# Optimization experiments

Measured on AMD Instinct MI355X. Metric: run time of the kernel, lower is better.

Reference implementation:

```python
import jax, jax.numpy as jnp
import numpy as np

N_NODES = 50000
N_EDGES = 800000
D_IN = 128
D_OUT = 128


def setup_inputs() -> dict:
    key = jax.random.key(0)
    k1, k2, k3, k4 = jax.random.split(key, 4)
    feature = jax.random.normal(k1, (N_NODES, D_IN), dtype=jnp.float32)
    relation_indices = jax.random.randint(k2, (2, N_EDGES), 0, N_NODES, dtype=jnp.int64)
    relation_weight = jax.random.uniform(k3, (N_EDGES, 1), dtype=jnp.float32)
    W = jax.random.normal(k4, (2 * D_IN, D_OUT), dtype=jnp.float32) * (1.0 / np.sqrt(2 * D_IN))
    b = jnp.zeros((D_OUT,), dtype=jnp.float32)
    return {"feature": feature, "relation_indices": relation_indices,
            "relation_weight": relation_weight, "W": W, "b": b}


def reference(feature, relation_indices, relation_weight, W, b):
    dst = relation_indices[0]  # segment ids (aggregation target) [E]
    src = relation_indices[1]  # neighbor ids gathered from feature [E]
    # gather neighbor features and apply edge weights (dropout_rate=0 -> identity)
    feat_n = feature[src] * relation_weight  # [E, D_IN]
    # segment mean over destination nodes
    n = feature.shape[0]
    sums = jax.ops.segment_sum(feat_n, dst, num_segments=n)  # [N, D_IN]
    cnts = jax.ops.segment_sum(jnp.ones((feat_n.shape[0],), dtype=feat_n.dtype), dst, num_segments=n)
    neigh_mean = sums / jnp.maximum(cnts, 1.0)[:, None]
    # concat(self, mean_neighbor) -> linear update
    h = jnp.concatenate([feature, neigh_mean], axis=-1)  # [N, 2*D_IN]
    return h @ W + b  # [N, D_OUT]
```

## Files before the change

### kernel.cpp

```cpp
#include <hip/hip_runtime.h>
#include <hip/hip_bf16.h>
#include <stdint.h>

#define N_NODES 50000
#define N_EDGES 800000
#define D 128
#define K_DIM 256
#define NB_SCAN 196

typedef __attribute__((ext_vector_type(8))) short bf16x8;
typedef __attribute__((ext_vector_type(4))) float f32x4;

#define SUMS_OFF  0
#define WSW_OFF   25600000
#define HIST_OFF  25665536
#define OFFS_OFF  25865536
#define CURS_OFF  26065552
#define EDGE_OFF  26265552
#define BSUM_OFF  32665552
#define BOFF_OFF  32666576

__device__ inline short f2bf(float x) {
  union { float f; uint32_t u; } v; v.f = x;
  uint32_t r = v.u + 0x7FFFu + ((v.u >> 16) & 1u);
  return (short)(r >> 16);
}

__global__ __launch_bounds__(256) void k_wswz(const float* __restrict__ W,
                                              short* __restrict__ wsw) {
  int t = blockIdx.x * 256 + threadIdx.x;
  int kstep = t >> 9;
  int ntile = (t >> 6) & 7;
  int lane  = t & 63;
  int k0  = kstep * 32 + (lane >> 4) * 8;
  int col = ntile * 16 + (lane & 15);
  bf16x8 o;
  #pragma unroll
  for (int j = 0; j < 8; ++j) o[j] = f2bf(W[(k0 + j) * D + col]);
  *(bf16x8*)(wsw + t * 8) = o;
}

__global__ __launch_bounds__(256) void k_hist(const int* __restrict__ idx,
                                              int* __restrict__ hist) {
  int e = blockIdx.x * 256 + threadIdx.x;
  if (e < N_EDGES) atomicAdd(&hist[idx[e]], 1);
}

__global__ __launch_bounds__(256) void k_scan1(const int* __restrict__ hist,
                                               int* __restrict__ blockSum) {
  __shared__ int red[256];
  int t = threadIdx.x;
  int i = blockIdx.x * 256 + t;
  red[t] = (i < N_NODES) ? hist[i] : 0;
  __syncthreads();
  #pragma unroll
  for (int s = 128; s > 0; s >>= 1) {
    if (t < s) red[t] += red[t + s];
    __syncthreads();
  }
  if (t == 0) blockSum[blockIdx.x] = red[0];
}

__global__ __launch_bounds__(256) void k_scan2(const int* __restrict__ blockSum,
                                               int* __restrict__ blockOff,
                                               int* __restrict__ offs) {
  __shared__ int lds[256];
  int t = threadIdx.x;
  int v = (t < NB_SCAN) ? blockSum[t] : 0;
  lds[t] = v;
  __syncthreads();
  #pragma unroll
  for (int off = 1; off < 256; off <<= 1) {
    int add = (t >= off) ? lds[t - off] : 0;
    __syncthreads();
    lds[t] += add;
    __syncthreads();
  }
  if (t < NB_SCAN) blockOff[t] = lds[t] - v;
  if (t == 255) offs[N_NODES] = lds[255];
}

__global__ __launch_bounds__(256) void k_scan3(const int* __restrict__ hist,
                                               const int* __restrict__ blockOff,
                                               int* __restrict__ offs,
                                               int* __restrict__ cursor) {
  __shared__ int lds[256];
  int t = threadIdx.x;
  int i = blockIdx.x * 256 + t;
  int v = (i < N_NODES) ? hist[i] : 0;
  lds[t] = v;
  __syncthreads();
  #pragma unroll
  for (int off = 1; off < 256; off <<= 1) {
    int add = (t >= off) ? lds[t - off] : 0;
    __syncthreads();
    lds[t] += add;
    __syncthreads();
  }
  int excl = lds[t] - v + blockOff[blockIdx.x];
  if (i < N_NODES) { offs[i] = excl; cursor[i] = excl; }
}

__global__ __launch_bounds__(256) void k_scatter(const int* __restrict__ idx,
                                                 const float* __restrict__ w,
                                                 int* __restrict__ cursor,
                                                 int2* __restrict__ edge) {
  int e = blockIdx.x * 256 + threadIdx.x;
  if (e < N_EDGES) {
    int dst = idx[e];
    int p = atomicAdd(&cursor[dst], 1);
    union { float f; int i; } u; u.f = w[e];
    edge[p] = make_int2(idx[N_EDGES + e], u.i);
  }
}

__global__ __launch_bounds__(256) void k_agg(const float* __restrict__ feat,
                                             const int* __restrict__ offs,
                                             const int2* __restrict__ edge,
                                             float* __restrict__ sums) {
  int t = blockIdx.x * 256 + threadIdx.x;
  int node = t >> 5;
  int c = t & 31;
  if (node >= N_NODES) return;
  int beg = offs[node], end = offs[node + 1];
  f32x4 acc = (f32x4){0.f, 0.f, 0.f, 0.f};
  for (int j = beg; j < end; ++j) {
    int2 ed = edge[j];
    union { int i; float f; } u; u.i = ed.y;
    float wt = u.f;
    f32x4 f = *(const f32x4*)(feat + (size_t)ed.x * D + c * 4);
    acc.x += f.x * wt; acc.y += f.y * wt; acc.z += f.z * wt; acc.w += f.w * wt;
  }
  *(f32x4*)(sums + (size_t)node * D + c * 4) = acc;
}

__global__ __launch_bounds__(256) void k_gemm(const float* __restrict__ feat,
                                              const float* __restrict__ sums,
                                              const int* __restrict__ offs,
                                              const short* __restrict__ wsw,
                                              const float* __restrict__ bias,
                                              float* __restrict__ out) {
  int wave = threadIdx.x >> 6;
  int lane = threadIdx.x & 63;
  int waveId = blockIdx.x * 4 + wave;
  int R = waveId * 16;
  if (R >= N_NODES) return;

  int row_l = lane & 15;
  int kq    = lane >> 4;
  int myrow = R + row_l;

  int deg = offs[myrow + 1] - offs[myrow];
  float invc = 1.0f / fmaxf((float)deg, 1.0f);

  f32x4 acc[8];
  #pragma unroll
  for (int nt = 0; nt < 8; ++nt) acc[nt] = (f32x4){0.f, 0.f, 0.f, 0.f};

  #pragma unroll
  for (int kstep = 0; kstep < 8; ++kstep) {
    int kbase = kstep * 32 + kq * 8;
    const float* srcrow;
    float scale;
    if (kstep < 4) { srcrow = feat + (size_t)myrow * D + kbase;        scale = 1.0f; }
    else           { srcrow = sums + (size_t)myrow * D + (kbase - D);  scale = invc; }
    f32x4 a0 = *(const f32x4*)(srcrow);
    f32x4 a1 = *(const f32x4*)(srcrow + 4);
    bf16x8 af;
    af[0] = f2bf(a0.x * scale); af[1] = f2bf(a0.y * scale);
    af[2] = f2bf(a0.z * scale); af[3] = f2bf(a0.w * scale);
    af[4] = f2bf(a1.x * scale); af[5] = f2bf(a1.y * scale);
    af[6] = f2bf(a1.z * scale); af[7] = f2bf(a1.w * scale);
    const bf16x8* wrow = (const bf16x8*)(wsw + ((size_t)kstep * 8 * 64 + lane) * 8);
    #pragma unroll
    for (int nt = 0; nt < 8; ++nt) {
      bf16x8 bf = wrow[nt * 64];
      acc[nt] = __builtin_amdgcn_mfma_f32_16x16x32_bf16(af, bf, acc[nt], 0, 0, 0);
    }
  }

  #pragma unroll
  for (int nt = 0; nt < 8; ++nt) {
    int col = nt * 16 + row_l;
    float bv = bias[col];
    #pragma unroll
    for (int r = 0; r < 4; ++r) {
      int orow = R + kq * 4 + r;
      out[(size_t)orow * D + col] = acc[nt][r] + bv;
    }
  }
}

extern "C" void kernel_launch(void* const* d_in, const int* in_sizes, int n_in,
                              void* d_out, int out_size, void* d_ws, size_t ws_size,
                              hipStream_t stream) {
  const float* feature = (const float*)d_in[0];
  const int*   rel_idx = (const int*)d_in[1];
  const float* rel_w   = (const float*)d_in[2];
  const float* W       = (const float*)d_in[3];
  const float* b       = (const float*)d_in[4];
  float* out = (float*)d_out;

  char* ws = (char*)d_ws;
  float* sums  = (float*)(ws + SUMS_OFF);
  short* wsw   = (short*)(ws + WSW_OFF);
  int*   hist  = (int*)(ws + HIST_OFF);
  int*   offs  = (int*)(ws + OFFS_OFF);
  int*   curs  = (int*)(ws + CURS_OFF);
  int2*  edge  = (int2*)(ws + EDGE_OFF);
  int*   bsum  = (int*)(ws + BSUM_OFF);
  int*   boff  = (int*)(ws + BOFF_OFF);

  hipMemsetAsync(hist, 0, N_NODES * sizeof(int), stream);
  k_wswz<<<16, 256, 0, stream>>>(W, wsw);
  k_hist<<<(N_EDGES + 255) / 256, 256, 0, stream>>>(rel_idx, hist);
  k_scan1<<<NB_SCAN, 256, 0, stream>>>(hist, bsum);
  k_scan2<<<1, 256, 0, stream>>>(bsum, boff, offs);
  k_scan3<<<NB_SCAN, 256, 0, stream>>>(hist, boff, offs, curs);
  k_scatter<<<(N_EDGES + 255) / 256, 256, 0, stream>>>(rel_idx, rel_w, curs, edge);
  k_agg<<<(N_NODES * 32 + 255) / 256, 256, 0, stream>>>(feature, offs, edge, sums);
  int gemmBlocks = (N_NODES / 16 + 3) / 4;
  k_gemm<<<gemmBlocks, 256, 0, stream>>>(feature, sums, offs, wsw, b, out);
}
```

Baseline: 257.3 us.

## Convert features to bf16 upfront and pack edges into 32-bit words

Adds a prep kernel that casts the feature matrix to bf16 and also takes over the histogram and W swizzle work, so one launch replaces three. Edges are packed as a 16-bit source index plus a bf16 weight, which halves the edge array. Aggregation now gathers bf16 rows using 64 threads per node, computes the mean, and writes it as bf16, so the GEMM reads bf16 operands directly. This cuts gather and GEMM memory traffic, at the cost of bf16 rounding of the weights and the gathered inputs. Storing the source index in 16 bits cannot represent node ids up to 50000 beyond 65535, which is fine here, but the packing is fragile.

Measured after the change: 263.1 us. 2.3% more time.

```diff
diff --git a/kernel.cpp b/kernel.cpp
--- a/kernel.cpp
+++ b/kernel.cpp
@@ -5,45 +5,62 @@
 #define N_NODES 50000
 #define N_EDGES 800000
 #define D 128
-#define K_DIM 256
 #define NB_SCAN 196
 
 typedef __attribute__((ext_vector_type(8))) short bf16x8;
 typedef __attribute__((ext_vector_type(4))) float f32x4;
-
-#define SUMS_OFF  0
-#define WSW_OFF   25600000
-#define HIST_OFF  25665536
-#define OFFS_OFF  25865536
-#define CURS_OFF  26065552
-#define EDGE_OFF  26265552
-#define BSUM_OFF  32665552
-#define BOFF_OFF  32666576
+typedef __attribute__((ext_vector_type(2))) short bf16x2;
+
+#define FEATBF_OFF 0
+#define MEANBF_OFF 12800000
+#define WSW_OFF    25600000
+#define HIST_OFF   25665536
+#define OFFS_OFF   25865536
+#define CURS_OFF   26065552
+#define EDGE_OFF   26265552
+#define BSUM_OFF   29465552
+#define BOFF_OFF   29466576
 
 __device__ inline short f2bf(float x) {
   union { float f; uint32_t u; } v; v.f = x;
   uint32_t r = v.u + 0x7FFFu + ((v.u >> 16) & 1u);
   return (short)(r >> 16);
 }
-
-__global__ __launch_bounds__(256) void k_wswz(const float* __restrict__ W,
+__device__ inline float bf2f(uint32_t bits16) {
+  union { uint32_t u; float f; } v; v.u = bits16 << 16;
+  return v.f;
+}
+
+__global__ __launch_bounds__(256) void k_prep(const float* __restrict__ feat,
+                                              const int* __restrict__ idx,
+                                              const float* __restrict__ W,
+                                              short* __restrict__ featbf,
+                                              int* __restrict__ hist,
                                               short* __restrict__ wsw) {
-  int t = blockIdx.x * 256 + threadIdx.x;
-  int kstep = t >> 9;
-  int ntile = (t >> 6) & 7;
-  int lane  = t & 63;
-  int k0  = kstep * 32 + (lane >> 4) * 8;
-  int col = ntile * 16 + (lane & 15);
-  bf16x8 o;
-  #pragma unroll
-  for (int j = 0; j < 8; ++j) o[j] = f2bf(W[(k0 + j) * D + col]);
-  *(bf16x8*)(wsw + t * 8) = o;
-}
-
-__global__ __launch_bounds__(256) void k_hist(const int* __restrict__ idx,
-                                              int* __restrict__ hist) {
-  int e = blockIdx.x * 256 + threadIdx.x;
-  if (e < N_EDGES) atomicAdd(&hist[idx[e]], 1);
+  int b = blockIdx.x;
+  if (b < 3125) {
+    int i = (b * 256 + threadIdx.x) * 8;
+    f32x4 a0 = *(const f32x4*)(feat + i);
+    f32x4 a1 = *(const f32x4*)(feat + i + 4);
+    bf16x8 o;
+    o[0] = f2bf(a0.x); o[1] = f2bf(a0.y); o[2] = f2bf(a0.z); o[3] = f2bf(a0.w);
+    o[4] = f2bf(a1.x); o[5] = f2bf(a1.y); o[6] = f2bf(a1.z); o[7] = f2bf(a1.w);
+    *(bf16x8*)(featbf + i) = o;
+  } else if (b < 6250) {
+    int e = (b - 3125) * 256 + threadIdx.x;
+    atomicAdd(&hist[idx[e]], 1);
+  } else {
+    int t = (b - 6250) * 256 + threadIdx.x;
+    int kstep = t >> 9;
+    int ntile = (t >> 6) & 7;
+    int lane  = t & 63;
+    int k0  = kstep * 32 + (lane >> 4) * 8;
+    int col = ntile * 16 + (lane & 15);
+    bf16x8 o;
+    #pragma unroll
+    for (int j = 0; j < 8; ++j) o[j] = f2bf(W[(k0 + j) * D + col]);
+    *(bf16x8*)(wsw + t * 8) = o;
+  }
 }
 
 __global__ __launch_bounds__(256) void k_scan1(const int* __restrict__ hist,
@@ -104,39 +121,44 @@
 __global__ __launch_bounds__(256) void k_scatter(const int* __restrict__ idx,
                                                  const float* __restrict__ w,
                                                  int* __restrict__ cursor,
-                                                 int2* __restrict__ edge) {
+                                                 uint32_t* __restrict__ edge) {
   int e = blockIdx.x * 256 + threadIdx.x;
   if (e < N_EDGES) {
     int dst = idx[e];
     int p = atomicAdd(&cursor[dst], 1);
-    union { float f; int i; } u; u.f = w[e];
-    edge[p] = make_int2(idx[N_EDGES + e], u.i);
-  }
-}
-
-__global__ __launch_bounds__(256) void k_agg(const float* __restrict__ feat,
+    uint32_t src = (uint32_t)idx[N_EDGES + e];
+    uint32_t wb  = (uint32_t)f2bf(w[e]) & 0xFFFFu;
+    edge[p] = (src << 16) | wb;
+  }
+}
+
+__global__ __launch_bounds__(256) void k_agg(const short* __restrict__ featbf,
                                              const int* __restrict__ offs,
-                                             const int2* __restrict__ edge,
-                                             float* __restrict__ sums) {
+                                             const uint32_t* __restrict__ edge,
+                                             short* __restrict__ meanbf) {
   int t = blockIdx.x * 256 + threadIdx.x;
-  int node = t >> 5;
-  int c = t & 31;
+  int node = t >> 6;
+  int c = t & 63;
   if (node >= N_NODES) return;
   int beg = offs[node], end = offs[node + 1];
-  f32x4 acc = (f32x4){0.f, 0.f, 0.f, 0.f};
+  float a0 = 0.f, a1 = 0.f;
   for (int j = beg; j < end; ++j) {
-    int2 ed = edge[j];
-    union { int i; float f; } u; u.i = ed.y;
-    float wt = u.f;
-    f32x4 f = *(const f32x4*)(feat + (size_t)ed.x * D + c * 4);
-    acc.x += f.x * wt; acc.y += f.y * wt; acc.z += f.z * wt; acc.w += f.w * wt;
-  }
-  *(f32x4*)(sums + (size_t)node * D + c * 4) = acc;
-}
-
-__global__ __launch_bounds__(256) void k_gemm(const float* __restrict__ feat,
-                                              const float* __restrict__ sums,
-                                              const int* __restrict__ offs,
+    uint32_t ed = edge[j];
+    float wt = bf2f(ed & 0xFFFFu);
+    uint32_t src = ed >> 16;
+    bf16x2 f = *(const bf16x2*)(featbf + (size_t)src * D + c * 2);
+    a0 += bf2f((uint16_t)f[0]) * wt;
+    a1 += bf2f((uint16_t)f[1]) * wt;
+  }
+  float invc = 1.0f / fmaxf((float)(end - beg), 1.0f);
+  bf16x2 o;
+  o[0] = f2bf(a0 * invc);
+  o[1] = f2bf(a1 * invc);
+  *(bf16x2*)(meanbf + (size_t)node * D + c * 2) = o;
+}
+
+__global__ __launch_bounds__(256) void k_gemm(const short* __restrict__ featbf,
+                                              const short* __restrict__ meanbf,
                                               const short* __restrict__ wsw,
                                               const float* __restrict__ bias,
                                               float* __restrict__ out) {
@@ -150,27 +172,16 @@
   int kq    = lane >> 4;
   int myrow = R + row_l;
 
-  int deg = offs[myrow + 1] - offs[myrow];
-  float invc = 1.0f / fmaxf((float)deg, 1.0f);
-
   f32x4 acc[8];
   #pragma unroll
   for (int nt = 0; nt < 8; ++nt) acc[nt] = (f32x4){0.f, 0.f, 0.f, 0.f};
 
   #pragma unroll
   for (int kstep = 0; kstep < 8; ++kstep) {
-    int kbase = kstep * 32 + kq * 8;
-    const float* srcrow;
-    float scale;
-    if (kstep < 4) { srcrow = feat + (size_t)myrow * D + kbase;        scale = 1.0f; }
-    else           { srcrow = sums + (size_t)myrow * D + (kbase - D);  scale = invc; }
-    f32x4 a0 = *(const f32x4*)(srcrow);
-    f32x4 a1 = *(const f32x4*)(srcrow + 4);
-    bf16x8 af;
-    af[0] = f2bf(a0.x * scale); af[1] = f2bf(a0.y * scale);
-    af[2] = f2bf(a0.z * scale); af[3] = f2bf(a0.w * scale);
-    af[4] = f2bf(a1.x * scale); af[5] = f2bf(a1.y * scale);
-    af[6] = f2bf(a1.z * scale); af[7] = f2bf(a1.w * scale);
+    int kbase = (kstep & 3) * 32 + kq * 8;
+    const short* srcrow = (kstep < 4) ? (featbf + (size_t)myrow * D + kbase)
+                                      : (meanbf + (size_t)myrow * D + kbase);
+    bf16x8 af = *(const bf16x8*)srcrow;
     const bf16x8* wrow = (const bf16x8*)(wsw + ((size_t)kstep * 8 * 64 + lane) * 8);
     #pragma unroll
     for (int nt = 0; nt < 8; ++nt) {
@@ -202,23 +213,23 @@
   float* out = (float*)d_out;
 
   char* ws = (char*)d_ws;
-  float* sums  = (float*)(ws + SUMS_OFF);
-  short* wsw   = (short*)(ws + WSW_OFF);
-  int*   hist  = (int*)(ws + HIST_OFF);
-  int*   offs  = (int*)(ws + OFFS_OFF);
-  int*   curs  = (int*)(ws + CURS_OFF);
-  int2*  edge  = (int2*)(ws + EDGE_OFF);
-  int*   bsum  = (int*)(ws + BSUM_OFF);
-  int*   boff  = (int*)(ws + BOFF_OFF);
+  short*    featbf = (short*)(ws + FEATBF_OFF);
+  short*    meanbf = (short*)(ws + MEANBF_OFF);
+  short*    wsw    = (short*)(ws + WSW_OFF);
+  int*      hist   = (int*)(ws + HIST_OFF);
+  int*      offs   = (int*)(ws + OFFS_OFF);
+  int*      curs   = (int*)(ws + CURS_OFF);
+  uint32_t* edge   = (uint32_t*)(ws + EDGE_OFF);
+  int*      bsum   = (int*)(ws + BSUM_OFF);
+  int*      boff   = (int*)(ws + BOFF_OFF);
 
   hipMemsetAsync(hist, 0, N_NODES * sizeof(int), stream);
-  k_wswz<<<16, 256, 0, stream>>>(W, wsw);
-  k_hist<<<(N_EDGES + 255) / 256, 256, 0, stream>>>(rel_idx, hist);
+  k_prep<<<6266, 256, 0, stream>>>(feature, rel_idx, W, featbf, hist, wsw);
   k_scan1<<<NB_SCAN, 256, 0, stream>>>(hist, bsum);
   k_scan2<<<1, 256, 0, stream>>>(bsum, boff, offs);
   k_scan3<<<NB_SCAN, 256, 0, stream>>>(hist, boff, offs, curs);
   k_scatter<<<(N_EDGES + 255) / 256, 256, 0, stream>>>(rel_idx, rel_w, curs, edge);
-  k_agg<<<(N_NODES * 32 + 255) / 256, 256, 0, stream>>>(feature, offs, edge, sums);
+  k_agg<<<(N_NODES * 64 + 255) / 256, 256, 0, stream>>>(featbf, offs, edge, meanbf);
   int gemmBlocks = (N_NODES / 16 + 3) / 4;
-  k_gemm<<<gemmBlocks, 256, 0, stream>>>(feature, sums, offs, wsw, b, out);
-}
+  k_gemm<<<gemmBlocks, 256, 0, stream>>>(featbf, meanbf, wsw, b, out);
+}
```
